# Kernel optimization log

Hardware: AMD Instinct MI355X
Metric: run time of the kernel (lower is better)

Reference implementation:

```python
import jax, jax.numpy as jnp
import numpy as np

B, N, F_IN, OUT_DIM, H = 8, 2048, 128, 256, 4
D = OUT_DIM // H  # head dim = 64
NEG_SLOPE = 0.2


def setup_inputs() -> dict:
    key = jax.random.key(0)
    k_a, k_x, k_w, k_s, k_d = jax.random.split(key, 5)
    A = jax.random.randint(k_a, (B, N, N), 0, 2).astype(jnp.float32)
    # ensure self-loops so no softmax row is fully masked (-inf -> NaN)
    eye = jnp.eye(N, dtype=jnp.float32)
    A = jnp.maximum(A, eye[None, :, :])
    X = jax.random.normal(k_x, (B, N, F_IN), dtype=jnp.float32)
    # xavier-uniform-like scales
    w_lim = float(np.sqrt(6.0 / (F_IN + OUT_DIM)))
    a_lim = float(np.sqrt(6.0 / (H + D)))
    W = jax.random.uniform(k_w, (OUT_DIM, F_IN), minval=-w_lim, maxval=w_lim, dtype=jnp.float32)
    a_src = jax.random.uniform(k_s, (H, D), minval=-a_lim, maxval=a_lim, dtype=jnp.float32)
    a_dst = jax.random.uniform(k_d, (H, D), minval=-a_lim, maxval=a_lim, dtype=jnp.float32)
    return {"A": A, "X": X, "W": W, "a_src": a_src, "a_dst": a_dst}


def reference(A, X, W, a_src, a_dst):
    b, n, _ = X.shape
    h, d = a_src.shape
    # X_trans = W(X); torch Linear: X @ W.T, W: (out_dim, in_dim)
    X_split = (X @ W.T).reshape(b, n, h, d)  # (b, n, h, d)
    attn_src = jnp.einsum('bnhd,hd->bnh', X_split, a_src)
    attn_dst = jnp.einsum('bnhd,hd->bnh', X_split, a_dst)
    # (b, n, n, h) dense score tensor
    attn = attn_src[:, :, None, :] + attn_dst[:, None, :, :]
    attn = jnp.where(attn >= 0, attn, NEG_SLOPE * attn)  # leaky_relu(0.2)
    attn = jnp.where(A[..., None] == 0, -jnp.inf, attn)
    attn = jax.nn.softmax(attn, axis=2)
    # torch.einsum('bnnk,bnkd->bnkd') with repeated 'n' -> DIAGONAL of attn,
    # elementwise-scaled features (faithful to original code).
    diag = jnp.einsum('bnnh->bnh', attn)  # (b, n, h): self-attention weights
    out = (diag[..., None] * X_split).reshape(b, n, h * d)
    return out
```

## Files before the change

kernel.cpp:

```cpp
#include <hip/hip_runtime.h>
#include <hip/hip_bf16.h>

#define B_   8
#define N_   2048
#define FIN  128
#define OUTD 256
#define H_   4
#define LOG2E 1.44269504088896340736f

typedef __bf16 bf16x8 __attribute__((ext_vector_type(8)));
typedef float  f32x4  __attribute__((ext_vector_type(4)));

__global__ __launch_bounds__(256) void conv_bf16(const float* __restrict__ X,
                                                 const float* __restrict__ W,
                                                 unsigned short* __restrict__ Xb,
                                                 unsigned short* __restrict__ Wb) {
    const int NX4 = (B_ * N_ * FIN) / 4;
    int i = blockIdx.x * 256 + threadIdx.x;
    const float4* src;
    ushort4* dst;
    int idx;
    if (i < NX4) { src = (const float4*)X; dst = (ushort4*)Xb; idx = i; }
    else         { src = (const float4*)W; dst = (ushort4*)Wb; idx = i - NX4; }
    float4 v = src[idx];
    __hip_bfloat16 b0 = __float2bfloat16(v.x);
    __hip_bfloat16 b1 = __float2bfloat16(v.y);
    __hip_bfloat16 b2 = __float2bfloat16(v.z);
    __hip_bfloat16 b3 = __float2bfloat16(v.w);
    ushort4 o;
    o.x = *(unsigned short*)&b0;
    o.y = *(unsigned short*)&b1;
    o.z = *(unsigned short*)&b2;
    o.w = *(unsigned short*)&b3;
    dst[idx] = o;
}

__global__ __launch_bounds__(256) void gemm_bf16(const unsigned short* __restrict__ Xb,
                                                 const unsigned short* __restrict__ Wb,
                                                 float* __restrict__ Xt) {
    int r0   = blockIdx.x * 16;
    int wave = threadIdx.x >> 6;
    int lane = threadIdx.x & 63;
    int c0   = (blockIdx.y * 4 + wave) * 16;
    int m = lane & 15, q = lane >> 4;

    const bf16x8* Arow = (const bf16x8*)(Xb + (size_t)(r0 + m) * FIN);
    const bf16x8* Brow = (const bf16x8*)(Wb + (size_t)(c0 + m) * FIN);
    f32x4 acc = {0.f, 0.f, 0.f, 0.f};
#pragma unroll
    for (int kc = 0; kc < 4; ++kc) {
        bf16x8 af = Arow[kc * 4 + q];
        bf16x8 bf = Brow[kc * 4 + q];
        acc = __builtin_amdgcn_mfma_f32_16x16x32_bf16(af, bf, acc, 0, 0, 0);
    }
    float* outp = Xt + (size_t)(r0 + q * 4) * OUTD + c0 + m;
#pragma unroll
    for (int reg = 0; reg < 4; ++reg)
        outp[(size_t)reg * OUTD] = acc[reg];
}

__global__ __launch_bounds__(256) void st_kernel(const float* __restrict__ Xt,
                                                 const float* __restrict__ a_src,
                                                 const float* __restrict__ a_dst,
                                                 float* __restrict__ s_arr,
                                                 float* __restrict__ t_arr) {
    int row  = blockIdx.x * 4 + (threadIdx.x >> 6);
    int lane = threadIdx.x & 63;
    f32x4 v  = ((const f32x4*)(Xt + (size_t)row * OUTD))[lane];
    f32x4 as = ((const f32x4*)a_src)[lane];
    f32x4 ad = ((const f32x4*)a_dst)[lane];

    float vs = fmaf(v[0], as[0], fmaf(v[1], as[1], fmaf(v[2], as[2], v[3] * as[3])));
    float vd = fmaf(v[0], ad[0], fmaf(v[1], ad[1], fmaf(v[2], ad[2], v[3] * ad[3])));
#pragma unroll
    for (int off = 1; off < 16; off <<= 1) {
        vs += __shfl_xor(vs, off);
        vd += __shfl_xor(vd, off);
    }
    if ((lane & 15) == 0) {
        int h = lane >> 4;
        s_arr[(size_t)row * H_ + h] = vs * LOG2E;
        t_arr[(size_t)row * H_ + h] = vd * LOG2E;
    }
}

__global__ __launch_bounds__(256) void gat_main(const float* __restrict__ A,
                                                const float* __restrict__ s_arr,
                                                const float* __restrict__ t_arr,
                                                float* __restrict__ out) {
    __shared__ float t_lds[N_ * H_];
    __shared__ float diag_lds[16][H_];

    int b  = blockIdx.x >> 7;
    int rt = blockIdx.x & 127;
    int r0 = rt * 16;
    int tid = threadIdx.x;

    {
        const float4* tsrc = (const float4*)(t_arr + (size_t)b * N_ * H_);
        float4* tdst = (float4*)t_lds;
#pragma unroll
        for (int i = 0; i < (N_ * H_) / 4 / 256; ++i)
            tdst[tid + i * 256] = tsrc[tid + i * 256];
    }
    __syncthreads();

    int r  = tid >> 4;
    int lj = tid & 15;
    int gi = r0 + r;

    f32x4 s4 = *(const f32x4*)(s_arr + ((size_t)b * N_ + gi) * H_);
    const float* Arow = A + ((size_t)b * N_ + gi) * N_;

    f32x4 acc = {0.f, 0.f, 0.f, 0.f};

    auto body = [&](float4 a4, int it) {
        int j = it * 64 + lj * 4;
#pragma unroll
        for (int jj = 0; jj < 4; ++jj) {
            f32x4 t4 = ((const f32x4*)t_lds)[j + jj];
            float aj = (jj == 0) ? a4.x : (jj == 1) ? a4.y : (jj == 2) ? a4.z : a4.w;
#pragma unroll
            for (int h = 0; h < H_; ++h) {
                float y = s4[h] + t4[h];
                y = fmaxf(y, 0.2f * y);
                acc[h] = fmaf(aj, __builtin_amdgcn_exp2f(y), acc[h]);
            }
        }
    };

    float4 a4 = *(const float4*)(Arow + lj * 4);
    for (int it = 0; it < 31; ++it) {
        float4 a4n = *(const float4*)(Arow + (it + 1) * 64 + lj * 4);
        body(a4, it);
        a4 = a4n;
    }
    body(a4, 31);

#pragma unroll
    for (int mk = 8; mk > 0; mk >>= 1) {
        acc[0] += __shfl_xor(acc[0], mk);
        acc[1] += __shfl_xor(acc[1], mk);
        acc[2] += __shfl_xor(acc[2], mk);
        acc[3] += __shfl_xor(acc[3], mk);
    }
    if (lj == 0) {
        f32x4 ti = ((const f32x4*)t_lds)[gi];
#pragma unroll
        for (int h = 0; h < H_; ++h) {
            float y = s4[h] + ti[h];
            y = fmaxf(y, 0.2f * y);
            diag_lds[r][h] = __builtin_amdgcn_exp2f(y) / acc[h];
        }
    }
    __syncthreads();

    float* orow = out + ((size_t)b * N_ + gi) * OUTD;
#pragma unroll
    for (int ii = 0; ii < 4; ++ii) {
        int c = lj * 4 + ii * 64;
        float4 v = *(float4*)(orow + c);
        float dg = diag_lds[r][ii];
        v.x *= dg; v.y *= dg; v.z *= dg; v.w *= dg;
        *(float4*)(orow + c) = v;
    }
}

extern "C" void kernel_launch(void* const* d_in, const int* in_sizes, int n_in,
                              void* d_out, int out_size, void* d_ws, size_t ws_size,
                              hipStream_t stream) {
    const float* A     = (const float*)d_in[0];
    const float* X     = (const float*)d_in[1];
    const float* W     = (const float*)d_in[2];
    const float* a_src = (const float*)d_in[3];
    const float* a_dst = (const float*)d_in[4];
    float* out = (float*)d_out;

    char* ws = (char*)d_ws;
    unsigned short* Xb = (unsigned short*)ws;
    unsigned short* Wb = (unsigned short*)(ws + 4194304);
    float* s_arr = (float*)(ws + 4259840);
    float* t_arr = (float*)(ws + 4521984);

    conv_bf16<<<2080, 256, 0, stream>>>(X, W, Xb, Wb);
    gemm_bf16<<<dim3(1024, 4), 256, 0, stream>>>(Xb, Wb, out);
    st_kernel<<<4096, 256, 0, stream>>>(out, a_src, a_dst, s_arr, t_arr);
    gat_main<<<1024, 256, 0, stream>>>(A, s_arr, t_arr, out);
}
```

Baseline: 236.4 us.

## Fuse bf16 conversion, projection GEMM and score dot-products into one kernel

Measured after the change: 234.1 us. Within noise of the previous version (-1.0%).

```diff
diff --git a/kernel.cpp b/kernel.cpp
--- a/kernel.cpp
+++ b/kernel.cpp
@@ -11,76 +11,79 @@
 typedef __bf16 bf16x8 __attribute__((ext_vector_type(8)));
 typedef float  f32x4  __attribute__((ext_vector_type(4)));
 
-__global__ __launch_bounds__(256) void conv_bf16(const float* __restrict__ X,
-                                                 const float* __restrict__ W,
-                                                 unsigned short* __restrict__ Xb,
-                                                 unsigned short* __restrict__ Wb) {
-    const int NX4 = (B_ * N_ * FIN) / 4;
-    int i = blockIdx.x * 256 + threadIdx.x;
-    const float4* src;
-    ushort4* dst;
-    int idx;
-    if (i < NX4) { src = (const float4*)X; dst = (ushort4*)Xb; idx = i; }
-    else         { src = (const float4*)W; dst = (ushort4*)Wb; idx = i - NX4; }
-    float4 v = src[idx];
-    __hip_bfloat16 b0 = __float2bfloat16(v.x);
-    __hip_bfloat16 b1 = __float2bfloat16(v.y);
-    __hip_bfloat16 b2 = __float2bfloat16(v.z);
-    __hip_bfloat16 b3 = __float2bfloat16(v.w);
-    ushort4 o;
-    o.x = *(unsigned short*)&b0;
-    o.y = *(unsigned short*)&b1;
-    o.z = *(unsigned short*)&b2;
-    o.w = *(unsigned short*)&b3;
-    dst[idx] = o;
+__device__ inline __bf16 cvt1(float f) {
+    __hip_bfloat16 b = __float2bfloat16(f);
+    return *reinterpret_cast<__bf16*>(&b);
 }
 
-__global__ __launch_bounds__(256) void gemm_bf16(const unsigned short* __restrict__ Xb,
-                                                 const unsigned short* __restrict__ Wb,
-                                                 float* __restrict__ Xt) {
+__global__ __launch_bounds__(256) void gemm_st(const float* __restrict__ X,
+                                               const float* __restrict__ W,
+                                               const float* __restrict__ a_src,
+                                               const float* __restrict__ a_dst,
+                                               float* __restrict__ Xt,
+                                               float* __restrict__ s_arr,
+                                               float* __restrict__ t_arr) {
     int r0   = blockIdx.x * 16;
-    int wave = threadIdx.x >> 6;
+    int h    = threadIdx.x >> 6;
     int lane = threadIdx.x & 63;
-    int c0   = (blockIdx.y * 4 + wave) * 16;
     int m = lane & 15, q = lane >> 4;
 
-    const bf16x8* Arow = (const bf16x8*)(Xb + (size_t)(r0 + m) * FIN);
-    const bf16x8* Brow = (const bf16x8*)(Wb + (size_t)(c0 + m) * FIN);
-    f32x4 acc = {0.f, 0.f, 0.f, 0.f};
+    const float* Arow = X + (size_t)(r0 + m) * FIN + q * 8;
+    f32x4 acc[4] = {{0,0,0,0},{0,0,0,0},{0,0,0,0},{0,0,0,0}};
+
 #pragma unroll
     for (int kc = 0; kc < 4; ++kc) {
-        bf16x8 af = Arow[kc * 4 + q];
-        bf16x8 bf = Brow[kc * 4 + q];
-        acc = __builtin_amdgcn_mfma_f32_16x16x32_bf16(af, bf, acc, 0, 0, 0);
+        float4 alo = *(const float4*)(Arow + kc * 32);
+        float4 ahi = *(const float4*)(Arow + kc * 32 + 4);
+        bf16x8 af;
+        af[0] = cvt1(alo.x); af[1] = cvt1(alo.y); af[2] = cvt1(alo.z); af[3] = cvt1(alo.w);
+        af[4] = cvt1(ahi.x); af[5] = cvt1(ahi.y); af[6] = cvt1(ahi.z); af[7] = cvt1(ahi.w);
+#pragma unroll
+        for (int ct = 0; ct < 4; ++ct) {
+            const float* Wrow = W + (size_t)(h * 64 + ct * 16 + m) * FIN + q * 8 + kc * 32;
+            float4 blo = *(const float4*)(Wrow);
+            float4 bhi = *(const float4*)(Wrow + 4);
+            bf16x8 bf;
+            bf[0] = cvt1(blo.x); bf[1] = cvt1(blo.y); bf[2] = cvt1(blo.z); bf[3] = cvt1(blo.w);
+            bf[4] = cvt1(bhi.x); bf[5] = cvt1(bhi.y); bf[6] = cvt1(bhi.z); bf[7] = cvt1(bhi.w);
+            acc[ct] = __builtin_amdgcn_mfma_f32_16x16x32_bf16(af, bf, acc[ct], 0, 0, 0);
+        }
     }
-    float* outp = Xt + (size_t)(r0 + q * 4) * OUTD + c0 + m;
+
 #pragma unroll
-    for (int reg = 0; reg < 4; ++reg)
-        outp[(size_t)reg * OUTD] = acc[reg];
-}
+    for (int ct = 0; ct < 4; ++ct) {
+        float* outp = Xt + (size_t)(r0 + q * 4) * OUTD + h * 64 + ct * 16 + m;
+#pragma unroll
+        for (int reg = 0; reg < 4; ++reg)
+            outp[(size_t)reg * OUTD] = acc[ct][reg];
+    }
 
-__global__ __launch_bounds__(256) void st_kernel(const float* __restrict__ Xt,
-                                                 const float* __restrict__ a_src,
-                                                 const float* __restrict__ a_dst,
-                                                 float* __restrict__ s_arr,
-                                                 float* __restrict__ t_arr) {
-    int row  = blockIdx.x * 4 + (threadIdx.x >> 6);
-    int lane = threadIdx.x & 63;
-    f32x4 v  = ((const f32x4*)(Xt + (size_t)row * OUTD))[lane];
-    f32x4 as = ((const f32x4*)a_src)[lane];
-    f32x4 ad = ((const f32x4*)a_dst)[lane];
-
-    float vs = fmaf(v[0], as[0], fmaf(v[1], as[1], fmaf(v[2], as[2], v[3] * as[3])));
-    float vd = fmaf(v[0], ad[0], fmaf(v[1], ad[1], fmaf(v[2], ad[2], v[3] * ad[3])));
+    float sp[4] = {0, 0, 0, 0}, tp[4] = {0, 0, 0, 0};
+#pragma unroll
+    for (int ct = 0; ct < 4; ++ct) {
+        float as = a_src[h * 64 + ct * 16 + m];
+        float ad = a_dst[h * 64 + ct * 16 + m];
+#pragma unroll
+        for (int reg = 0; reg < 4; ++reg) {
+            sp[reg] = fmaf(acc[ct][reg], as, sp[reg]);
+            tp[reg] = fmaf(acc[ct][reg], ad, tp[reg]);
+        }
+    }
 #pragma unroll
     for (int off = 1; off < 16; off <<= 1) {
-        vs += __shfl_xor(vs, off);
-        vd += __shfl_xor(vd, off);
+#pragma unroll
+        for (int reg = 0; reg < 4; ++reg) {
+            sp[reg] += __shfl_xor(sp[reg], off);
+            tp[reg] += __shfl_xor(tp[reg], off);
+        }
     }
-    if ((lane & 15) == 0) {
-        int h = lane >> 4;
-        s_arr[(size_t)row * H_ + h] = vs * LOG2E;
-        t_arr[(size_t)row * H_ + h] = vd * LOG2E;
+    if (m == 0) {
+#pragma unroll
+        for (int reg = 0; reg < 4; ++reg) {
+            size_t row = (size_t)(r0 + q * 4 + reg);
+            s_arr[row * H_ + h] = sp[reg] * LOG2E;
+            t_arr[row * H_ + h] = tp[reg] * LOG2E;
+        }
     }
 }
 
@@ -121,10 +124,10 @@
             f32x4 t4 = ((const f32x4*)t_lds)[j + jj];
             float aj = (jj == 0) ? a4.x : (jj == 1) ? a4.y : (jj == 2) ? a4.z : a4.w;
 #pragma unroll
-            for (int h = 0; h < H_; ++h) {
-                float y = s4[h] + t4[h];
+            for (int hh = 0; hh < H_; ++hh) {
+                float y = s4[hh] + t4[hh];
                 y = fmaxf(y, 0.2f * y);
-                acc[h] = fmaf(aj, __builtin_amdgcn_exp2f(y), acc[h]);
+                acc[hh] = fmaf(aj, __builtin_amdgcn_exp2f(y), acc[hh]);
             }
         }
     };
@@ -147,10 +150,10 @@
     if (lj == 0) {
         f32x4 ti = ((const f32x4*)t_lds)[gi];
 #pragma unroll
-        for (int h = 0; h < H_; ++h) {
-            float y = s4[h] + ti[h];
+        for (int hh = 0; hh < H_; ++hh) {
+            float y = s4[hh] + ti[hh];
             y = fmaxf(y, 0.2f * y);
-            diag_lds[r][h] = __builtin_amdgcn_exp2f(y) / acc[h];
+            diag_lds[r][hh] = __builtin_amdgcn_exp2f(y) / acc[hh];
         }
     }
     __syncthreads();
@@ -177,13 +180,9 @@
     float* out = (float*)d_out;
 
     char* ws = (char*)d_ws;
-    unsigned short* Xb = (unsigned short*)ws;
-    unsigned short* Wb = (unsigned short*)(ws + 4194304);
-    float* s_arr = (float*)(ws + 4259840);
-    float* t_arr = (float*)(ws + 4521984);
+    float* s_arr = (float*)ws;
+    float* t_arr = (float*)(ws + 262144);
 
-    conv_bf16<<<2080, 256, 0, stream>>>(X, W, Xb, Wb);
-    gemm_bf16<<<dim3(1024, 4), 256, 0, stream>>>(Xb, Wb, out);
-    st_kernel<<<4096, 256, 0, stream>>>(out, a_src, a_dst, s_arr, t_arr);
+    gemm_st<<<1024, 256, 0, stream>>>(X, W, a_src, a_dst, out, s_arr, t_arr);
     gat_main<<<1024, 256, 0, stream>>>(A, s_arr, t_arr, out);
 }
```
